# Performance work log

Measured on AMD Instinct MI355X. Metric: run time of the kernel, lower is better.

## Reference

```python
import jax, jax.numpy as jnp
import numpy as np

F8_MAX = 448.0  # float8_e4m3fn max
F4_MAX = 6.0    # fp4 e2m1 max
BLOCK = 16      # NVFP4 scaling block size along K

# representable |values| of fp4 e2m1 and midpoints for nearest rounding
_LEVELS = jnp.array([0.0, 0.5, 1.0, 1.5, 2.0, 3.0, 4.0, 6.0], dtype=jnp.float32)
_MIDS = (_LEVELS[:-1] + _LEVELS[1:]) * 0.5


def _e2m1_round(a):
    # round-to-nearest fp4 e2m1 value, sign-magnitude
    s = jnp.sign(a)
    m = jnp.clip(jnp.abs(a), 0.0, F4_MAX)
    idx = jnp.searchsorted(_MIDS, m, side='left')
    return s * jnp.take(_LEVELS, idx)


def _e4m3(x):
    # quantize to float8 e4m3 and dequantize back to fp32
    return jnp.clip(x, -F8_MAX, F8_MAX).astype(jnp.float8_e4m3fn).astype(jnp.float32)


def nvfp4_fake_quant(x, s2):
    # x: [..., K]; s2: scalar global scale = 448*6/global_amax
    shp = x.shape
    K = shp[-1]
    xb = x.reshape(shp[:-1] + (K // BLOCK, BLOCK))  # [..., K/16, 16]
    amax = jnp.max(jnp.abs(xb), axis=-1, keepdims=True)
    sf = _e4m3(amax * s2 / F4_MAX)          # stored per-block fp8 scale (cutlass_vec)
    scale = sf / s2                          # per-block dequant scale in real units
    safe = jnp.where(scale > 0.0, scale, 1.0)
    q = _e2m1_round(xb / safe)               # fp4 codes (as values)
    deq = jnp.where(scale > 0.0, q * scale, 0.0)
    return deq.reshape(shp)


def setup_inputs() -> dict:
    key = jax.random.key(0)
    kx, kw, kb, ks = jax.random.split(key, 4)
    K, N = 4096, 4096
    x = jax.random.normal(kx, (4, 2048, K), dtype=jnp.float32)
    weight = jax.random.uniform(kw, (N, K), dtype=jnp.float32)
    bias = jax.random.uniform(kb, (N,), dtype=jnp.float32)
    # fp4_global_scale of a rand(1, K) tensor, as done in the module __init__
    dummy = jax.random.uniform(ks, (1, K), dtype=jnp.float32)
    s_in2 = ((F8_MAX * F4_MAX) / jnp.max(jnp.abs(dummy))).reshape(1)
    return {'x': x, 'weight': weight, 'bias': bias, 's_in2': s_in2}


def reference(x, weight, bias, s_in2):
    s2_in = s_in2.reshape(())
    s2_w = (F8_MAX * F4_MAX) / jnp.max(jnp.abs(weight))  # fp4_global_scale(weight)
    x_dq = nvfp4_fake_quant(x, s2_in)        # fake-quant activations
    w_dq = nvfp4_fake_quant(weight, s2_w)    # dequantized fp4 weight (stored at init)
    # F.linear: [b,s,k] @ [n,k]^T + bias
    return jnp.einsum('bsk,nk->bsn', x_dq, w_dq) + bias
```

## Files before the change

### kernel.cpp

```cpp
#include <hip/hip_runtime.h>
#include <hip/hip_bf16.h>

typedef __attribute__((ext_vector_type(8))) short short8;
typedef __attribute__((ext_vector_type(8))) unsigned short ushort8;
typedef __attribute__((ext_vector_type(4))) float f32x4;
typedef unsigned short ushort;

#define K_DIM 4096
#define N_DIM 4096
#define BK 32
#define NT (K_DIM / BK)


__device__ __forceinline__ float e4m3_rne(float v) {
    if (v >= 0.015625f) {
        unsigned u = __float_as_uint(v);
        unsigned lsb = (u >> 20) & 1u;
        u = (u + 0x7FFFFu + lsb) & 0xFFF00000u;
        return __uint_as_float(u);
    }
    return rintf(v * 512.0f) * 0.001953125f;
}

__device__ __forceinline__ float e2m1_level(float m) {
    float lv = 0.0f;
    lv = (m > 0.25f) ? 0.5f : lv;
    lv = (m > 0.75f) ? 1.0f : lv;
    lv = (m > 1.25f) ? 1.5f : lv;
    lv = (m > 1.75f) ? 2.0f : lv;
    lv = (m > 2.5f)  ? 3.0f : lv;
    lv = (m > 3.5f)  ? 4.0f : lv;
    lv = (m > 5.0f)  ? 6.0f : lv;
    return lv;
}

__device__ __forceinline__ ushort f32_to_bf16_bits(float f) {
    unsigned u = __float_as_uint(f);
    return (ushort)((u + 0x7FFFu + ((u >> 16) & 1u)) >> 16);
}


__global__ void wamax_kernel(const float* __restrict__ w, unsigned* amax_bits, int n4) {
    float m = 0.f;
    const f32x4* w4 = (const f32x4*)w;
    for (int i = blockIdx.x * blockDim.x + threadIdx.x; i < n4; i += gridDim.x * blockDim.x) {
        f32x4 v = w4[i];
        m = fmaxf(m, fmaxf(fmaxf(fabsf(v.x), fabsf(v.y)), fmaxf(fabsf(v.z), fabsf(v.w))));
    }
#pragma unroll
    for (int off = 32; off >= 1; off >>= 1)
        m = fmaxf(m, __shfl_down(m, off));
    __shared__ float red[4];
    const int lane = threadIdx.x & 63, wv = threadIdx.x >> 6;
    if (lane == 0) red[wv] = m;
    __syncthreads();
    if (threadIdx.x == 0) {
        m = fmaxf(fmaxf(red[0], red[1]), fmaxf(red[2], red[3]));
        atomicMax(amax_bits, __float_as_uint(m));
    }
}

__global__ void quant16_kernel(const float* __restrict__ src,
                               const float* __restrict__ s2_ptr,
                               const unsigned* __restrict__ amax_bits,
                               ushort* __restrict__ dst, int nblk) {
    int t = blockIdx.x * blockDim.x + threadIdx.x;
    if (t >= nblk) return;
    float s2;
    if (s2_ptr) s2 = *s2_ptr;
    else        s2 = 2688.0f / __uint_as_float(*amax_bits);

    const f32x4* s = (const f32x4*)src + (size_t)t * 4;
    float vals[16];
    f32x4 v0 = s[0], v1 = s[1], v2 = s[2], v3 = s[3];
#pragma unroll
    for (int i = 0; i < 4; ++i) {
        vals[i] = v0[i]; vals[4 + i] = v1[i]; vals[8 + i] = v2[i]; vals[12 + i] = v3[i];
    }
    float amax = 0.f;
#pragma unroll
    for (int i = 0; i < 16; ++i) amax = fmaxf(amax, fabsf(vals[i]));

    float sf = e4m3_rne(fminf(amax * s2 / 6.0f, 448.0f));
    float scale = sf / s2;

    ushort8 o0, o1;
    if (scale > 0.f) {
#pragma unroll
        for (int i = 0; i < 16; ++i) {
            float r = vals[i] / scale;
            float m = fminf(fabsf(r), 6.0f);
            float q = copysignf(e2m1_level(m), r);
            ushort b = f32_to_bf16_bits(q * scale);
            if (i < 8) o0[i] = b; else o1[i - 8] = b;
        }
    } else {
#pragma unroll
        for (int i = 0; i < 8; ++i) { o0[i] = 0; o1[i] = 0; }
    }
    ushort8* d8 = (ushort8*)(dst + (size_t)t * 16);
    d8[0] = o0;
    d8[1] = o1;
}


__device__ __forceinline__ void gload16(const ushort* g, ushort* l) {
    __builtin_amdgcn_global_load_lds(
        (const __attribute__((address_space(1))) void*)g,
        (__attribute__((address_space(3))) void*)l, 16, 0, 0);
}

#define VM4 asm volatile("s_waitcnt vmcnt(4)" ::: "memory")
#define VM0 asm volatile("s_waitcnt vmcnt(0)" ::: "memory")
#define LG4 do { asm volatile("s_waitcnt lgkmcnt(4)" ::: "memory"); \
                 __builtin_amdgcn_sched_barrier(0); } while (0)
#define LG0 do { asm volatile("s_waitcnt lgkmcnt(0)" ::: "memory"); \
                 __builtin_amdgcn_sched_barrier(0); } while (0)
#define BAR asm volatile("s_barrier" ::: "memory")

__global__ __launch_bounds__(512, 2) void gemm8(
    const ushort* __restrict__ Aq, const ushort* __restrict__ Bq,
    const float* __restrict__ bias, float* __restrict__ C) {
    __shared__ ushort lds[4 * 16384];

    const int tid  = threadIdx.x;
    const int lane = tid & 63;
    const int wave = tid >> 6;
    const int wr = wave >> 2;
    const int wc = wave & 3;

    const int swz = blockIdx.x;
    const int grp = swz >> 8, lcl = swz & 255;
    const int by = grp * 16 + (lcl & 15);
    const int bx = lcl >> 4;
    const int bm = by * 256, bn = bx * 256;

    const int r0  = tid >> 2;
    const int cg0 = ((tid & 3) - ((r0 >> 1) & 3)) & 3;
    const ushort* sA0 = Aq + (size_t)(bm + r0) * K_DIM + cg0 * 8;
    const ushort* sB0 = Bq + (size_t)(bn + r0) * K_DIM + cg0 * 8;
    ushort* dA0 = &lds[wave * 512];
    ushort* dB0 = &lds[8192 + wave * 512];

    const int pr   = ((lane >> 4) + ((lane & 15) >> 1)) & 3;
    const int idxA = (wr * 128 + (lane & 15)) * 32 + pr * 8;
    const int idxB = 8192 + (wc * 64 + (lane & 15)) * 32 + pr * 8;

    f32x4 acc[8][4];
#pragma unroll
    for (int m = 0; m < 8; ++m)
#pragma unroll
        for (int n = 0; n < 4; ++n) acc[m][n] = (f32x4)(0.f);

    short8 af[8], bfr[4];

#define SA(t) { const size_t ko = (size_t)(t) * BK; const int bb = ((t) & 3) * 16384; \
    gload16(sA0 + ko, dA0 + bb); gload16(sA0 + (size_t)128 * K_DIM + ko, dA0 + bb + 4096); }
#define SB(t) { const size_t ko = (size_t)(t) * BK; const int bb = ((t) & 3) * 16384; \
    gload16(sB0 + ko, dB0 + bb); gload16(sB0 + (size_t)128 * K_DIM + ko, dB0 + bb + 4096); }

#define READ_ALO(bb) _Pragma("unroll") for (int m = 0; m < 4; ++m) \
        af[m] = *(const short8*)&lds[(bb) + idxA + m * 512];
#define READ_AHI(bb) _Pragma("unroll") for (int m = 0; m < 4; ++m) \
        af[4 + m] = *(const short8*)&lds[(bb) + idxA + (4 + m) * 512];
#define READ_B(bb)   _Pragma("unroll") for (int n = 0; n < 4; ++n) \
        bfr[n] = *(const short8*)&lds[(bb) + idxB + n * 512];

#define MML                                                                   \
    __builtin_amdgcn_s_setprio(1);                                            \
    _Pragma("unroll") for (int m = 0; m < 4; ++m)                             \
    _Pragma("unroll") for (int n = 0; n < 4; ++n)                             \
        acc[m][n] = __builtin_amdgcn_mfma_f32_16x16x32_bf16(af[m], bfr[n], acc[m][n], 0, 0, 0); \
    __builtin_amdgcn_s_setprio(0);
#define MMH                                                                   \
    __builtin_amdgcn_s_setprio(1);                                            \
    _Pragma("unroll") for (int m = 4; m < 8; ++m)                             \
    _Pragma("unroll") for (int n = 0; n < 4; ++n)                             \
        acc[m][n] = __builtin_amdgcn_mfma_f32_16x16x32_bf16(af[m], bfr[n], acc[m][n], 0, 0, 0); \
    __builtin_amdgcn_s_setprio(0);

    SA(0); SB(0); SA(1); SB(1); SA(2); SB(2);
    VM4; BAR;
    READ_ALO(0); READ_B(0);

#pragma unroll 1
    for (int t = 0; t <= NT - 4; ++t) {
        const int bb  = (t & 3) * 16384;
        const int bb1 = ((t + 1) & 3) * 16384;
        VM4; BAR;
        READ_AHI(bb);
        SA(t + 3);
        LG4;
        MML;
        READ_ALO(bb1);
        SB(t + 3);
        LG4;
        MMH;
        READ_B(bb1);
    }
    {
        const int bb  = ((NT - 3) & 3) * 16384;
        const int bb1 = ((NT - 2) & 3) * 16384;
        VM4; BAR;
        READ_AHI(bb);
        LG4; MML;
        READ_ALO(bb1);
        LG4; MMH;
        READ_B(bb1);
    }
    {
        const int bb  = ((NT - 2) & 3) * 16384;
        const int bb1 = ((NT - 1) & 3) * 16384;
        VM0; BAR;
        READ_AHI(bb);
        LG4; MML;
        READ_ALO(bb1);
        LG4; MMH;
        READ_B(bb1);
    }
    {
        const int bb = ((NT - 1) & 3) * 16384;
        READ_AHI(bb);
        LG4; MML;
        LG0; MMH;
    }

    const int fq = lane >> 4, fr = lane & 15;
    float bv[4];
#pragma unroll
    for (int n = 0; n < 4; ++n) bv[n] = bias[bn + wc * 64 + n * 16 + fr];
#pragma unroll
    for (int m = 0; m < 8; ++m)
#pragma unroll
        for (int r = 0; r < 4; ++r) {
            const int row = bm + wr * 128 + m * 16 + fq * 4 + r;
            float* Cr = C + (size_t)row * N_DIM + bn + wc * 64 + fr;
#pragma unroll
            for (int n = 0; n < 4; ++n) Cr[n * 16] = acc[m][n][r] + bv[n];
        }
#undef SA
#undef SB
#undef READ_ALO
#undef READ_AHI
#undef READ_B
#undef MML
#undef MMH
}


extern "C" void kernel_launch(void* const* d_in, const int* in_sizes, int n_in,
                              void* d_out, int out_size, void* d_ws, size_t ws_size,
                              hipStream_t stream) {
    const float* x     = (const float*)d_in[0];
    const float* w     = (const float*)d_in[1];
    const float* bias  = (const float*)d_in[2];
    const float* s_in2 = (const float*)d_in[3];
    float* out = (float*)d_out;

    const int M = in_sizes[0] / K_DIM;

    unsigned* amax_bits = (unsigned*)d_ws;
    ushort* xq = (ushort*)((char*)d_ws + 256);
    ushort* wq = (ushort*)((char*)d_ws + 256 + (size_t)M * K_DIM * 2);

    hipMemsetAsync(amax_bits, 0, 4, stream);
    wamax_kernel<<<1024, 256, 0, stream>>>(w, amax_bits, (N_DIM * K_DIM) / 4);

    const int nblk_x = (M * K_DIM) / 16;
    quant16_kernel<<<nblk_x / 256, 256, 0, stream>>>(x, s_in2, nullptr, xq, nblk_x);
    const int nblk_w = (N_DIM * K_DIM) / 16;
    quant16_kernel<<<nblk_w / 256, 256, 0, stream>>>(w, nullptr, amax_bits, wq, nblk_w);

    const int nwg = (M / 256) * (N_DIM / 256);
    gemm8<<<nwg, 512, 0, stream>>>(xq, wq, bias, out);
}
```

Measured before the change: 297.7 us.

## Merge activation and weight quant kernels and drop explicit LDS waitcounts

Fuses the two per-block quantization launches into one kernel that picks the source tensor and scale from the thread index, saving one launch and its tail. It also removes the hand-placed lgkmcnt waits and sched barriers between LDS reads and MFMA groups in the GEMM main loop, leaving wait insertion to the compiler. That gives the compiler more scheduling freedom but can lose the intended interleaving of LDS reads with MFMAs.

```diff
diff --git a/kernel.cpp b/kernel.cpp
--- a/kernel.cpp
+++ b/kernel.cpp
@@ -60,15 +60,23 @@
     }
 }
 
-__global__ void quant16_kernel(const float* __restrict__ src,
-                               const float* __restrict__ s2_ptr,
-                               const unsigned* __restrict__ amax_bits,
-                               ushort* __restrict__ dst, int nblk) {
+__global__ void quant_both_kernel(const float* __restrict__ x,
+                                  const float* __restrict__ w,
+                                  const float* __restrict__ s2_ptr,
+                                  const unsigned* __restrict__ amax_bits,
+                                  ushort* __restrict__ xq,
+                                  ushort* __restrict__ wq, int nx, int ntot) {
     int t = blockIdx.x * blockDim.x + threadIdx.x;
-    if (t >= nblk) return;
+    if (t >= ntot) return;
+    const float* src;
+    ushort* dst;
     float s2;
-    if (s2_ptr) s2 = *s2_ptr;
-    else        s2 = 2688.0f / __uint_as_float(*amax_bits);
+    if (t < nx) {
+        src = x; dst = xq; s2 = *s2_ptr;
+    } else {
+        src = w; dst = wq; t -= nx;
+        s2 = 2688.0f / __uint_as_float(*amax_bits);
+    }
 
     const f32x4* s = (const f32x4*)src + (size_t)t * 4;
     float vals[16];
@@ -112,10 +120,6 @@
 
 #define VM4 asm volatile("s_waitcnt vmcnt(4)" ::: "memory")
 #define VM0 asm volatile("s_waitcnt vmcnt(0)" ::: "memory")
-#define LG4 do { asm volatile("s_waitcnt lgkmcnt(4)" ::: "memory"); \
-                 __builtin_amdgcn_sched_barrier(0); } while (0)
-#define LG0 do { asm volatile("s_waitcnt lgkmcnt(0)" ::: "memory"); \
-                 __builtin_amdgcn_sched_barrier(0); } while (0)
 #define BAR asm volatile("s_barrier" ::: "memory")
 
 __global__ __launch_bounds__(512, 2) void gemm8(
@@ -190,11 +194,9 @@
         VM4; BAR;
         READ_AHI(bb);
         SA(t + 3);
-        LG4;
         MML;
         READ_ALO(bb1);
         SB(t + 3);
-        LG4;
         MMH;
         READ_B(bb1);
     }
@@ -203,9 +205,9 @@
         const int bb1 = ((NT - 2) & 3) * 16384;
         VM4; BAR;
         READ_AHI(bb);
-        LG4; MML;
+        MML;
         READ_ALO(bb1);
-        LG4; MMH;
+        MMH;
         READ_B(bb1);
     }
     {
@@ -213,16 +215,16 @@
         const int bb1 = ((NT - 1) & 3) * 16384;
         VM0; BAR;
         READ_AHI(bb);
-        LG4; MML;
+        MML;
         READ_ALO(bb1);
-        LG4; MMH;
+        MMH;
         READ_B(bb1);
     }
     {
         const int bb = ((NT - 1) & 3) * 16384;
         READ_AHI(bb);
-        LG4; MML;
-        LG0; MMH;
+        MML;
+        MMH;
     }
 
     const int fq = lane >> 4, fr = lane & 15;
@@ -266,10 +268,10 @@
     hipMemsetAsync(amax_bits, 0, 4, stream);
     wamax_kernel<<<1024, 256, 0, stream>>>(w, amax_bits, (N_DIM * K_DIM) / 4);
 
-    const int nblk_x = (M * K_DIM) / 16;
-    quant16_kernel<<<nblk_x / 256, 256, 0, stream>>>(x, s_in2, nullptr, xq, nblk_x);
-    const int nblk_w = (N_DIM * K_DIM) / 16;
-    quant16_kernel<<<nblk_w / 256, 256, 0, stream>>>(w, nullptr, amax_bits, wq, nblk_w);
+    const int nx = (M * K_DIM) / 16;
+    const int nw = (N_DIM * K_DIM) / 16;
+    quant_both_kernel<<<(nx + nw) / 256, 256, 0, stream>>>(
+        x, w, s_in2, amax_bits, xq, wq, nx, nx + nw);
 
     const int nwg = (M / 256) * (N_DIM / 256);
     gemm8<<<nwg, 512, 0, stream>>>(xq, wq, bias, out);
```

After: 291.1 us, median of 2. -2.2%, faster.
